# Optimization experiments

Measured on AMD Instinct MI355X. Metric: run time of the kernel, lower is better.

The kernel has to match this reference:

```python
import jax, jax.numpy as jnp
import numpy as np

N_NODES = 100000
N_EDGES = 1600000
IN_DIM, H1, H2, OUT_DIM = 128, 64, 64, 64


def _glorot(key, shape):
    fan_in, fan_out = shape
    lim = np.sqrt(6.0 / (fan_in + fan_out)).astype(np.float32)
    return jax.random.uniform(key, shape, jnp.float32, -lim, lim)


def setup_inputs() -> dict:
    key = jax.random.key(0)
    ks = jax.random.split(key, 8)
    x = jax.random.normal(ks[0], (N_NODES, IN_DIM), jnp.float32)
    edge_index = jax.random.randint(ks[1], (2, N_EDGES), 0, N_NODES, jnp.int64)
    W1 = _glorot(ks[2], (IN_DIM, H1))
    b1 = jnp.zeros((H1,), jnp.float32)
    W2 = _glorot(ks[3], (H1, H2))
    b2 = jnp.zeros((H2,), jnp.float32)
    Wfc = _glorot(ks[4], (H2, OUT_DIM))
    bfc = jnp.zeros((OUT_DIM,), jnp.float32)
    return {"x": x, "W1": W1, "b1": b1, "W2": W2, "b2": b2,
            "Wfc": Wfc, "bfc": bfc, "edge_index": edge_index}


def _gcn_conv(x, src, dst, dinv, W, b, n_nodes):
    # PyG GCNConv: h = D^{-1/2} (A + I) D^{-1/2} (x W) + b
    h = x @ W                                   # [N, out]
    norm = dinv[src] * dinv[dst]                # [E'] edge weights
    msg = norm[:, None] * h[src]                # gather + scale, [E', out]
    agg = jax.ops.segment_sum(msg, dst, num_segments=n_nodes)
    return agg + b


def reference(x, W1, b1, W2, b2, Wfc, bfc, edge_index):
    n = x.shape[0]
    loop = jnp.arange(n, dtype=edge_index.dtype)
    src = jnp.concatenate([edge_index[0], loop])   # self-loops appended
    dst = jnp.concatenate([edge_index[1], loop])
    deg = jnp.zeros((n,), x.dtype).at[dst].add(1.0)  # degree incl. self-loop
    dinv = jax.lax.rsqrt(deg)

    h = jax.nn.relu(_gcn_conv(x, src, dst, dinv, W1, b1, n))
    h = jax.nn.relu(_gcn_conv(h, src, dst, dinv, W2, b2, n))
    embedding = h
    logits = h @ Wfc + bfc
    return embedding, logits
```

## Files before the change

### kernel.cpp

```cpp
#include <hip/hip_runtime.h>
#include <hip/hip_bf16.h>


constexpr int IN_DIM  = 128;
constexpr int HDIM    = 64;
constexpr int NBLK_A  = 256;
constexpr int BSH     = 8;
constexpr int MAXNB   = 512;

__device__ __forceinline__ float bf2f(unsigned int u) {
    return __uint_as_float(u << 16);
}
__device__ __forceinline__ unsigned short f2bf_bits(float f) {
    __hip_bfloat16 b = __float2bfloat16(f);
    return *(unsigned short*)&b;
}


__global__ void binA_count(const int* __restrict__ dst, int* __restrict__ histg,
                           int E, int NB, int chunk) {
    __shared__ int h[MAXNB];
    for (int i = threadIdx.x; i < NB; i += 256) h[i] = 0;
    __syncthreads();
    int beg = blockIdx.x * chunk;
    int end = min(E, beg + chunk);
    for (int e = beg + threadIdx.x; e < end; e += 256)
        atomicAdd(&h[dst[e] >> BSH], 1);
    __syncthreads();
    for (int i = threadIdx.x; i < NB; i += 256)
        histg[i * NBLK_A + blockIdx.x] = h[i];
}

__global__ void binA_scanblocks(int* __restrict__ histg, int* __restrict__ btot) {
    __shared__ int sm[NBLK_A];
    int tid = threadIdx.x;
    int v = histg[blockIdx.x * NBLK_A + tid];
    sm[tid] = v;
    __syncthreads();
    for (int off = 1; off < NBLK_A; off <<= 1) {
        int t = (tid >= off) ? sm[tid - off] : 0;
        __syncthreads();
        sm[tid] += t;
        __syncthreads();
    }
    histg[blockIdx.x * NBLK_A + tid] = sm[tid] - v;
    if (tid == NBLK_A - 1) btot[blockIdx.x] = sm[tid];
}

__global__ void binA_scanbuckets(const int* __restrict__ btot, int* __restrict__ bucketbase,
                                 int NB) {
    __shared__ int sm[MAXNB];
    int tid = threadIdx.x;
    int v = (tid < NB) ? btot[tid] : 0;
    sm[tid] = v;
    __syncthreads();
    for (int off = 1; off < MAXNB; off <<= 1) {
        int t = (tid >= off) ? sm[tid - off] : 0;
        __syncthreads();
        sm[tid] += t;
        __syncthreads();
    }
    if (tid < NB) bucketbase[tid] = sm[tid] - v;
    if (tid == MAXNB - 1) bucketbase[NB] = sm[tid];
}

__global__ void binA_scatter(const int* __restrict__ src, const int* __restrict__ dst,
                             const int* __restrict__ histg, const int* __restrict__ bucketbase,
                             int* __restrict__ staging, int E, int NB, int chunk) {
    __shared__ int cur[MAXNB];
    for (int i = threadIdx.x; i < NB; i += 256)
        cur[i] = bucketbase[i] + histg[i * NBLK_A + blockIdx.x];
    __syncthreads();
    int beg = blockIdx.x * chunk;
    int end = min(E, beg + chunk);
    for (int e = beg + threadIdx.x; e < end; e += 256) {
        int s = src[e];
        int d = dst[e];
        int pos = atomicAdd(&cur[d >> BSH], 1);
        staging[pos] = (s << BSH) | (d & 255);
    }
}

__global__ void binB_finalize(const int* __restrict__ staging, const int* __restrict__ bucketbase,
                              int* __restrict__ rowptr, int* __restrict__ esrc,
                              float* __restrict__ dinv, int N, int NB) {
    __shared__ int cnt[256], sm[256], cur[256];
    int tid = threadIdx.x;
    int b = blockIdx.x;
    int node0 = b << BSH;
    int nloc = min(256, N - node0);
    int ebeg = bucketbase[b], eend = bucketbase[b + 1];
    cnt[tid] = 0;
    __syncthreads();
    for (int e = ebeg + tid; e < eend; e += 256)
        atomicAdd(&cnt[staging[e] & 255], 1);
    __syncthreads();
    int v = cnt[tid];
    sm[tid] = v;
    __syncthreads();
    for (int off = 1; off < 256; off <<= 1) {
        int t = (tid >= off) ? sm[tid - off] : 0;
        __syncthreads();
        sm[tid] += t;
        __syncthreads();
    }
    int excl = sm[tid] - v;
    cur[tid] = excl;
    __syncthreads();
    if (tid < nloc) {
        rowptr[node0 + tid] = ebeg + excl;
        dinv[node0 + tid] = rsqrtf((float)v + 1.0f);
    }
    if (b == 0 && tid == 0) rowptr[N] = bucketbase[NB];
    for (int e = ebeg + tid; e < eend; e += 256) {
        int p = staging[e];
        int pos = ebeg + atomicAdd(&cur[p & 255], 1);
        esrc[pos] = p >> BSH;
    }
}


template<int K, bool IBF16, bool SCALE, bool BIAS, bool OBF16>
__device__ __forceinline__ void gemm_body(
        const void* __restrict__ Xv, const float* __restrict__ W,
        const float* __restrict__ bias, const float* __restrict__ dinv,
        void* __restrict__ Yv, int n) {
    constexpr int KC = 32;
    constexpr int XSTR = 132;
    __shared__ float Xt[KC * XSTR];
    __shared__ float Ws[KC * 64];
    const int tid = threadIdx.x;
    const int node0 = blockIdx.x * 128;
    const int r0 = (tid >> 4) * 8;
    const int c0 = (tid & 15) * 4;

    float acc[8][4];
#pragma unroll
    for (int a = 0; a < 8; ++a)
#pragma unroll
        for (int b = 0; b < 4; ++b) acc[a][b] = 0.f;

    for (int kc = 0; kc < K; kc += KC) {
        __syncthreads();
#pragma unroll
        for (int i = 0; i < 4; ++i) {
            int s = tid + i * 256;
            int row = s >> 3;
            int kq = s & 7;
            int grow = node0 + row;
            float4 v = make_float4(0.f, 0.f, 0.f, 0.f);
            if (grow < n) {
                if (IBF16) {
                    uint2 u = *(const uint2*)&((const unsigned short*)Xv)[(size_t)grow * K + kc + kq * 4];
                    v.x = bf2f(u.x & 0xffff); v.y = bf2f(u.x >> 16);
                    v.z = bf2f(u.y & 0xffff); v.w = bf2f(u.y >> 16);
                } else {
                    v = *(const float4*)&((const float*)Xv)[(size_t)grow * K + kc + kq * 4];
                }
            }
            Xt[(kq * 4 + 0) * XSTR + row] = v.x;
            Xt[(kq * 4 + 1) * XSTR + row] = v.y;
            Xt[(kq * 4 + 2) * XSTR + row] = v.z;
            Xt[(kq * 4 + 3) * XSTR + row] = v.w;
        }
#pragma unroll
        for (int i = 0; i < 2; ++i) {
            int s = tid + i * 256;
            *(float4*)&Ws[s * 4] = *(const float4*)&W[(size_t)kc * 64 + s * 4];
        }
        __syncthreads();
#pragma unroll
        for (int kk = 0; kk < KC; kk += 4) {
            float4 xa[4][2];
            float4 wv[4];
#pragma unroll
            for (int i = 0; i < 4; ++i) {
                xa[i][0] = *(const float4*)&Xt[(kk + i) * XSTR + r0];
                xa[i][1] = *(const float4*)&Xt[(kk + i) * XSTR + r0 + 4];
                wv[i]    = *(const float4*)&Ws[(kk + i) * 64 + c0];
            }
#pragma unroll
            for (int i = 0; i < 4; ++i) {
                const float* xp = (const float*)&xa[i][0];
                const float* wp = (const float*)&wv[i];
#pragma unroll
                for (int rr = 0; rr < 8; ++rr)
#pragma unroll
                    for (int cc = 0; cc < 4; ++cc)
                        acc[rr][cc] += xp[rr] * wp[cc];
            }
        }
    }
#pragma unroll
    for (int rr = 0; rr < 8; ++rr) {
        int node = node0 + r0 + rr;
        if (node < n) {
            float d = SCALE ? dinv[node] : 1.0f;
            float t[4];
#pragma unroll
            for (int cc = 0; cc < 4; ++cc) {
                float v = acc[rr][cc];
                if (BIAS) v += bias[c0 + cc];
                t[cc] = v * d;
            }
            if (OBF16) {
                __hip_bfloat16 vb[4];
#pragma unroll
                for (int cc = 0; cc < 4; ++cc) vb[cc] = __float2bfloat16(t[cc]);
                *(uint2*)&((__hip_bfloat16*)Yv)[(size_t)node * 64 + c0] = *(uint2*)vb;
            } else {
                *(float4*)&((float*)Yv)[(size_t)node * 64 + c0] = *(float4*)t;
            }
        }
    }
}

__global__ __launch_bounds__(256, 4) void gemm1_kernel(
        const float* X, const float* W, const float* dinv, void* Y, int n) {
    gemm_body<IN_DIM, false, true, false, true>(X, W, nullptr, dinv, Y, n);
}
__global__ __launch_bounds__(256, 4) void gemm2_kernel(
        const void* X, const float* W, const float* dinv, void* Y, int n) {
    gemm_body<HDIM, true, true, false, true>(X, W, nullptr, dinv, Y, n);
}
__global__ __launch_bounds__(256, 4) void fc_kernel(
        const float* X, const float* W, const float* bias, void* Y, int n) {
    gemm_body<HDIM, false, false, true, false>(X, W, bias, nullptr, Y, n);
}

template<bool OBF16>
__device__ __forceinline__ void agg_body(
        const unsigned short* __restrict__ hp, const int* __restrict__ esrc,
        const int* __restrict__ rowptr, const float* __restrict__ dinv,
        const float* __restrict__ bias, void* __restrict__ out, int n) {
    int node = blockIdx.x * 4 + (threadIdx.x >> 6);
    if (node >= n) return;
    int lane = threadIdx.x & 63;
    int half = lane >> 5;
    int l = lane & 31;
    const unsigned int* hp32 = (const unsigned int*)hp;
    int beg = rowptr[node], end = rowptr[node + 1];

    float ax = 0.f, ay = 0.f;
    {
        unsigned int u = hp32[(size_t)node * 32 + l];
        if (half == 0) { ax = bf2f(u & 0xffff); ay = bf2f(u >> 16); }
    }
    int k = beg;
    for (; k + 16 <= end; k += 16) {
        int s[8];
#pragma unroll
        for (int i = 0; i < 8; ++i) s[i] = esrc[k + 2 * i + half];
        unsigned int u[8];
#pragma unroll
        for (int i = 0; i < 8; ++i) u[i] = hp32[(size_t)s[i] * 32 + l];
        float vx[8], vy[8];
#pragma unroll
        for (int i = 0; i < 8; ++i) { vx[i] = bf2f(u[i] & 0xffff); vy[i] = bf2f(u[i] >> 16); }
        ax += ((vx[0] + vx[1]) + (vx[2] + vx[3])) + ((vx[4] + vx[5]) + (vx[6] + vx[7]));
        ay += ((vy[0] + vy[1]) + (vy[2] + vy[3])) + ((vy[4] + vy[5]) + (vy[6] + vy[7]));
    }
    if (k < end) {
        int s[8];
#pragma unroll
        for (int i = 0; i < 8; ++i) s[i] = esrc[min(k + 2 * i + half, end - 1)];
        unsigned int u[8];
#pragma unroll
        for (int i = 0; i < 8; ++i) u[i] = hp32[(size_t)s[i] * 32 + l];
        float tx = 0.f, ty = 0.f;
#pragma unroll
        for (int i = 0; i < 8; ++i) {
            bool m = (k + 2 * i + half) < end;
            tx += m ? bf2f(u[i] & 0xffff) : 0.f;
            ty += m ? bf2f(u[i] >> 16)    : 0.f;
        }
        ax += tx; ay += ty;
    }
    ax += __shfl_xor(ax, 32, 64);
    ay += __shfl_xor(ay, 32, 64);

    if (half == 0) {
        float d = dinv[node];
        float ox = fmaxf(d * ax + bias[2 * l], 0.f);
        float oy = fmaxf(d * ay + bias[2 * l + 1], 0.f);
        if (OBF16) {
            unsigned int packed = (unsigned int)f2bf_bits(ox) | ((unsigned int)f2bf_bits(oy) << 16);
            ((unsigned int*)out)[(size_t)node * 32 + l] = packed;
        } else {
            float2 o = make_float2(ox, oy);
            ((float2*)out)[(size_t)node * 32 + l] = o;
        }
    }
}

__global__ __launch_bounds__(256) void agg1_kernel(
        const unsigned short* hp, const int* esrc, const int* rowptr,
        const float* dinv, const float* bias, void* out, int n) {
    agg_body<true>(hp, esrc, rowptr, dinv, bias, out, n);
}
__global__ __launch_bounds__(256) void agg2_kernel(
        const unsigned short* hp, const int* esrc, const int* rowptr,
        const float* dinv, const float* bias, void* out, int n) {
    agg_body<false>(hp, esrc, rowptr, dinv, bias, out, n);
}

extern "C" void kernel_launch(void* const* d_in, const int* in_sizes, int n_in,
                              void* d_out, int out_size, void* d_ws, size_t ws_size,
                              hipStream_t stream) {
    const float* x   = (const float*)d_in[0];
    const float* W1  = (const float*)d_in[1];
    const float* b1  = (const float*)d_in[2];
    const float* W2  = (const float*)d_in[3];
    const float* b2  = (const float*)d_in[4];
    const float* Wfc = (const float*)d_in[5];
    const float* bfc = (const float*)d_in[6];
    const int*  eidx = (const int*)d_in[7];

    const int N = in_sizes[0] / IN_DIM;
    const int E = in_sizes[7] / 2;
    const int* src = eidx;
    const int* dst = eidx + E;

    const int NB    = (N + 255) >> BSH;
    const int chunk = (E + NBLK_A - 1) / NBLK_A;

    int*   rowptr     = (int*)d_ws;
    float* dinv       = (float*)(rowptr + (N + 2));
    int*   histg      = (int*)(dinv + N);
    int*   btot       = histg + (size_t)NB * NBLK_A + (((size_t)NB * NBLK_A) & 1);
    int*   bucketbase = btot + 512;
    int*   esrc       = bucketbase + 512;
    float* bufA       = (float*)(esrc + E + (E & 1));
    float* bufB       = bufA + (size_t)N * HDIM;
    int*   staging    = (int*)bufA;
    unsigned short* hp = (unsigned short*)bufA;
    unsigned short* h1 = (unsigned short*)bufB;

    float* emb    = (float*)d_out;
    float* logits = emb + (size_t)N * HDIM;

    binA_count<<<NBLK_A, 256, 0, stream>>>(dst, histg, E, NB, chunk);
    binA_scanblocks<<<NB, NBLK_A, 0, stream>>>(histg, btot);
    binA_scanbuckets<<<1, MAXNB, 0, stream>>>(btot, bucketbase, NB);
    binA_scatter<<<NBLK_A, 256, 0, stream>>>(src, dst, histg, bucketbase, staging, E, NB, chunk);
    binB_finalize<<<NB, 256, 0, stream>>>(staging, bucketbase, rowptr, esrc, dinv, N, NB);

    const int gBlocks = (N + 127) / 128;
    const int aBlocks = (N + 3) / 4;

    gemm1_kernel<<<gBlocks, 256, 0, stream>>>(x, W1, dinv, hp, N);
    agg1_kernel<<<aBlocks, 256, 0, stream>>>(hp, esrc, rowptr, dinv, b1, h1, N);

    gemm2_kernel<<<gBlocks, 256, 0, stream>>>(h1, W2, dinv, hp, N);
    agg2_kernel<<<aBlocks, 256, 0, stream>>>(hp, esrc, rowptr, dinv, b2, emb, N);

    fc_kernel<<<gBlocks, 256, 0, stream>>>(emb, Wfc, bfc, logits, N);
}
```

Before: 315.8 us.

## Replace FP32 SIMT GEMMs with bf16 MFMA 16x16x32 matrix-core kernels

Rewrites the three dense GEMM kernels (layer-1 transform, layer-2 transform, final FC) to use the bf16 16x16x32 MFMA instruction. Each wave computes 16 rows by 64 columns, loading A fragments straight from global memory and converting fp32 inputs to bf16 in registers. W is transposed and converted to bf16 in shared memory by every block. This removes the FP32 FMA inner loop and its shared-memory staging of X, but every block now rebuilds W, the output stores are narrow scalar writes, and it adds bf16 rounding to x and to the fp32 embedding fed to the FC layer.

Result: slower. 323.4 us (+2.4%).

```diff
diff --git a/kernel.cpp b/kernel.cpp
--- a/kernel.cpp
+++ b/kernel.cpp
@@ -7,6 +7,9 @@
 constexpr int NBLK_A  = 256;
 constexpr int BSH     = 8;
 constexpr int MAXNB   = 512;
+
+typedef __attribute__((ext_vector_type(8))) short short8;
+typedef __attribute__((ext_vector_type(4))) float floatx4;
 
 __device__ __forceinline__ float bf2f(unsigned int u) {
     return __uint_as_float(u << 16);
@@ -121,112 +124,90 @@
 
 
 template<int K, bool IBF16, bool SCALE, bool BIAS, bool OBF16>
-__device__ __forceinline__ void gemm_body(
+__device__ __forceinline__ void mfma_gemm_body(
         const void* __restrict__ Xv, const float* __restrict__ W,
         const float* __restrict__ bias, const float* __restrict__ dinv,
         void* __restrict__ Yv, int n) {
-    constexpr int KC = 32;
-    constexpr int XSTR = 132;
-    __shared__ float Xt[KC * XSTR];
-    __shared__ float Ws[KC * 64];
+    constexpr int KP = K + 8;
+    __shared__ unsigned short Wt[64 * KP];
     const int tid = threadIdx.x;
-    const int node0 = blockIdx.x * 128;
-    const int r0 = (tid >> 4) * 8;
-    const int c0 = (tid & 15) * 4;
-
-    float acc[8][4];
-#pragma unroll
-    for (int a = 0; a < 8; ++a)
-#pragma unroll
-        for (int b = 0; b < 4; ++b) acc[a][b] = 0.f;
-
-    for (int kc = 0; kc < K; kc += KC) {
-        __syncthreads();
-#pragma unroll
-        for (int i = 0; i < 4; ++i) {
-            int s = tid + i * 256;
-            int row = s >> 3;
-            int kq = s & 7;
-            int grow = node0 + row;
-            float4 v = make_float4(0.f, 0.f, 0.f, 0.f);
-            if (grow < n) {
-                if (IBF16) {
-                    uint2 u = *(const uint2*)&((const unsigned short*)Xv)[(size_t)grow * K + kc + kq * 4];
-                    v.x = bf2f(u.x & 0xffff); v.y = bf2f(u.x >> 16);
-                    v.z = bf2f(u.y & 0xffff); v.w = bf2f(u.y >> 16);
-                } else {
-                    v = *(const float4*)&((const float*)Xv)[(size_t)grow * K + kc + kq * 4];
-                }
-            }
-            Xt[(kq * 4 + 0) * XSTR + row] = v.x;
-            Xt[(kq * 4 + 1) * XSTR + row] = v.y;
-            Xt[(kq * 4 + 2) * XSTR + row] = v.z;
-            Xt[(kq * 4 + 3) * XSTR + row] = v.w;
-        }
-#pragma unroll
-        for (int i = 0; i < 2; ++i) {
-            int s = tid + i * 256;
-            *(float4*)&Ws[s * 4] = *(const float4*)&W[(size_t)kc * 64 + s * 4];
-        }
-        __syncthreads();
-#pragma unroll
-        for (int kk = 0; kk < KC; kk += 4) {
-            float4 xa[4][2];
-            float4 wv[4];
-#pragma unroll
-            for (int i = 0; i < 4; ++i) {
-                xa[i][0] = *(const float4*)&Xt[(kk + i) * XSTR + r0];
-                xa[i][1] = *(const float4*)&Xt[(kk + i) * XSTR + r0 + 4];
-                wv[i]    = *(const float4*)&Ws[(kk + i) * 64 + c0];
-            }
-#pragma unroll
-            for (int i = 0; i < 4; ++i) {
-                const float* xp = (const float*)&xa[i][0];
-                const float* wp = (const float*)&wv[i];
-#pragma unroll
-                for (int rr = 0; rr < 8; ++rr)
-#pragma unroll
-                    for (int cc = 0; cc < 4; ++cc)
-                        acc[rr][cc] += xp[rr] * wp[cc];
-            }
-        }
-    }
-#pragma unroll
-    for (int rr = 0; rr < 8; ++rr) {
-        int node = node0 + r0 + rr;
+    for (int i = tid; i < K * 64; i += 256) {
+        int k = i % K, c = i / K;
+        Wt[c * KP + k] = f2bf_bits(W[k * 64 + c]);
+    }
+    __syncthreads();
+
+    const int wid  = tid >> 6;
+    const int lane = tid & 63;
+    const int q    = lane >> 4;
+    const int m    = lane & 15;
+    const int rbase = blockIdx.x * 64 + wid * 16;
+    int lrow = rbase + m;
+    if (lrow > n - 1) lrow = n - 1;
+
+    short8 a[K / 32];
+#pragma unroll
+    for (int c = 0; c < K / 32; ++c) {
+        if (IBF16) {
+            a[c] = *(const short8*)((const unsigned short*)Xv + (size_t)lrow * K + c * 32 + q * 8);
+        } else {
+            const float* xp = (const float*)Xv + (size_t)lrow * K + c * 32 + q * 8;
+            floatx4 f0 = *(const floatx4*)xp;
+            floatx4 f1 = *(const floatx4*)(xp + 4);
+            short8 t;
+            t[0] = (short)f2bf_bits(f0[0]); t[1] = (short)f2bf_bits(f0[1]);
+            t[2] = (short)f2bf_bits(f0[2]); t[3] = (short)f2bf_bits(f0[3]);
+            t[4] = (short)f2bf_bits(f1[0]); t[5] = (short)f2bf_bits(f1[1]);
+            t[6] = (short)f2bf_bits(f1[2]); t[7] = (short)f2bf_bits(f1[3]);
+            a[c] = t;
+        }
+    }
+
+    floatx4 acc[4];
+#pragma unroll
+    for (int nt = 0; nt < 4; ++nt) acc[nt] = (floatx4){0.f, 0.f, 0.f, 0.f};
+
+#pragma unroll
+    for (int c = 0; c < K / 32; ++c) {
+#pragma unroll
+        for (int nt = 0; nt < 4; ++nt) {
+            short8 b = *(const short8*)&Wt[(nt * 16 + m) * KP + c * 32 + q * 8];
+            acc[nt] = __builtin_amdgcn_mfma_f32_16x16x32_bf16(a[c], b, acc[nt], 0, 0, 0);
+        }
+    }
+
+#pragma unroll
+    for (int r = 0; r < 4; ++r) {
+        int node = rbase + q * 4 + r;
         if (node < n) {
             float d = SCALE ? dinv[node] : 1.0f;
-            float t[4];
-#pragma unroll
-            for (int cc = 0; cc < 4; ++cc) {
-                float v = acc[rr][cc];
-                if (BIAS) v += bias[c0 + cc];
-                t[cc] = v * d;
+#pragma unroll
+            for (int nt = 0; nt < 4; ++nt) {
+                float v = acc[nt][r];
+                if (BIAS) v += bias[nt * 16 + m];
+                v *= d;
+                if (OBF16)
+                    ((unsigned short*)Yv)[(size_t)node * 64 + nt * 16 + m] = f2bf_bits(v);
+                else
+                    ((float*)Yv)[(size_t)node * 64 + nt * 16 + m] = v;
             }
-            if (OBF16) {
-                __hip_bfloat16 vb[4];
-#pragma unroll
-                for (int cc = 0; cc < 4; ++cc) vb[cc] = __float2bfloat16(t[cc]);
-                *(uint2*)&((__hip_bfloat16*)Yv)[(size_t)node * 64 + c0] = *(uint2*)vb;
-            } else {
-                *(float4*)&((float*)Yv)[(size_t)node * 64 + c0] = *(float4*)t;
-            }
-        }
-    }
-}
-
-__global__ __launch_bounds__(256, 4) void gemm1_kernel(
+        }
+    }
+}
+
+__global__ __launch_bounds__(256) void gemm1_kernel(
         const float* X, const float* W, const float* dinv, void* Y, int n) {
-    gemm_body<IN_DIM, false, true, false, true>(X, W, nullptr, dinv, Y, n);
-}
-__global__ __launch_bounds__(256, 4) void gemm2_kernel(
+    mfma_gemm_body<IN_DIM, false, true, false, true>(X, W, nullptr, dinv, Y, n);
+}
+__global__ __launch_bounds__(256) void gemm2_kernel(
         const void* X, const float* W, const float* dinv, void* Y, int n) {
-    gemm_body<HDIM, true, true, false, true>(X, W, nullptr, dinv, Y, n);
-}
-__global__ __launch_bounds__(256, 4) void fc_kernel(
+    mfma_gemm_body<HDIM, true, true, false, true>(X, W, nullptr, dinv, Y, n);
+}
+__global__ __launch_bounds__(256) void fc_kernel(
         const float* X, const float* W, const float* bias, void* Y, int n) {
-    gemm_body<HDIM, false, false, true, false>(X, W, bias, nullptr, Y, n);
-}
+    mfma_gemm_body<HDIM, false, false, true, false>(X, W, bias, nullptr, Y, n);
+}
+
 
 template<bool OBF16>
 __device__ __forceinline__ void agg_body(
@@ -270,9 +251,9 @@
         float tx = 0.f, ty = 0.f;
 #pragma unroll
         for (int i = 0; i < 8; ++i) {
-            bool m = (k + 2 * i + half) < end;
-            tx += m ? bf2f(u[i] & 0xffff) : 0.f;
-            ty += m ? bf2f(u[i] >> 16)    : 0.f;
+            bool mm = (k + 2 * i + half) < end;
+            tx += mm ? bf2f(u[i] & 0xffff) : 0.f;
+            ty += mm ? bf2f(u[i] >> 16)    : 0.f;
         }
         ax += tx; ay += ty;
     }
@@ -287,8 +268,7 @@
             unsigned int packed = (unsigned int)f2bf_bits(ox) | ((unsigned int)f2bf_bits(oy) << 16);
             ((unsigned int*)out)[(size_t)node * 32 + l] = packed;
         } else {
-            float2 o = make_float2(ox, oy);
-            ((float2*)out)[(size_t)node * 32 + l] = o;
+            ((float2*)out)[(size_t)node * 32 + l] = make_float2(ox, oy);
         }
     }
 }
@@ -345,7 +325,7 @@
     binA_scatter<<<NBLK_A, 256, 0, stream>>>(src, dst, histg, bucketbase, staging, E, NB, chunk);
     binB_finalize<<<NB, 256, 0, stream>>>(staging, bucketbase, rowptr, esrc, dinv, N, NB);
 
-    const int gBlocks = (N + 127) / 128;
+    const int gBlocks = (N + 63) / 64;
     const int aBlocks = (N + 3) / 4;
 
     gemm1_kernel<<<gBlocks, 256, 0, stream>>>(x, W1, dinv, hp, N);
```
